# Optimization experiments

Hardware: AMD Instinct MI355X
Metric: run time of the kernel (lower is better)

Reference implementation:

```python
import jax, jax.numpy as jnp
import numpy as np
import math

B = 4096
D = 768
HID = 256
C_OLD = 100
C_NEW = 100
NUM_CLASSES = 200
EPSILON = 0.05
TAU = 0.1
EPS = 1e-8
NEG_INF = -1e9


def _l2_normalize(x):
    # matches F.normalize(p=2, dim=1, eps=1e-12)
    n = jnp.linalg.norm(x, axis=1, keepdims=True)
    return x / jnp.maximum(n, 1e-12)


def setup_inputs() -> dict:
    key = jax.random.key(0)
    k1, k2, k3, k4, k5, k6, k7 = jax.random.split(key, 7)
    z_u = jax.random.normal(k1, (B, D), dtype=jnp.float32)
    logits = jax.random.normal(k2, (B, NUM_CLASSES), dtype=jnp.float32)
    old_class_indices = jnp.arange(C_OLD, dtype=jnp.int64 if jax.config.jax_enable_x64 else jnp.int32)
    new_class_indices = jnp.arange(C_OLD, C_OLD + C_NEW, dtype=old_class_indices.dtype)
    base_features = jax.random.normal(k3, (B, D), dtype=jnp.float32)
    s = 1.0 / math.sqrt(D)
    f1_w = jax.random.uniform(k4, (HID, D), dtype=jnp.float32, minval=-s, maxval=s)
    f1_b = jax.random.uniform(k5, (HID,), dtype=jnp.float32, minval=-s, maxval=s)
    f2_w = jax.random.uniform(k6, (HID, D), dtype=jnp.float32, minval=-s, maxval=s)
    f2_b = jax.random.uniform(k7, (HID,), dtype=jnp.float32, minval=-s, maxval=s)
    return {"z_u": z_u, "logits": logits, "old_class_indices": old_class_indices,
            "new_class_indices": new_class_indices, "base_features": base_features,
            "f1_w": f1_w, "f1_b": f1_b, "f2_w": f2_w, "f2_b": f2_b}


def reference(z_u, logits, old_class_indices, new_class_indices, base_features,
              f1_w, f1_b, f2_w, f2_b):
    num_old = old_class_indices.shape[0]
    active = jnp.concatenate([old_class_indices, new_class_indices])

    # ---- soft entropy regularization ----
    probs = jax.nn.softmax(logits[:, active], axis=1)   # (B, C_old+C_new)
    mean_probs = probs.mean(axis=0)
    p_old = mean_probs[:num_old].sum()
    p_new = mean_probs[num_old:].sum()
    loss_inter = (p_old * jnp.log(p_old + EPS) + p_new * jnp.log(p_new + EPS)
                  + math.log(2.0))
    p_old_in = mean_probs[:num_old] / (p_old + EPS)
    loss_old_in = jnp.sum(p_old_in * jnp.log(p_old_in + EPS)) + math.log(num_old)
    p_new_in = mean_probs[num_old:] / (p_new + EPS)
    num_new = new_class_indices.shape[0]
    if num_new > 1:
        loss_new_in = jnp.sum(p_new_in * jnp.log(p_new_in + EPS)) + math.log(num_new)
    else:
        loss_new_in = jnp.float32(0.0)
    loss_entropy = loss_inter + loss_old_in + loss_new_in

    # ---- neighborhood mask from frozen base features ----
    base_norm = _l2_normalize(base_features)
    base_sim = base_norm @ base_norm.T                  # (B, B)
    eye = jnp.eye(base_sim.shape[0], dtype=bool)
    mask = (base_sim > EPSILON) & ~eye                  # (B, B) bool

    # ---- contrastive similarities ----
    z_norm = _l2_normalize(z_u)
    sim = z_norm @ z_norm.T                             # (B, B)

    f1_z = z_u @ f1_w.T + f1_b                          # (B, HID)
    f2_z = z_u @ f2_w.T + f2_b
    attn_logits = jnp.where(mask, f1_z @ f2_z.T, NEG_INF)
    w_ik = jax.nn.softmax(attn_logits, axis=1) * mask.astype(sim.dtype)

    exp_sim = jnp.where(eye, 0.0, jnp.exp(sim / TAU))
    denom = exp_sim.sum(axis=1, keepdims=True)
    log_prob = sim / TAU - jnp.log(denom + EPS)

    num_neighbors = mask.sum(axis=1).astype(sim.dtype)  # (B,)
    valid = num_neighbors > 0
    loss_i = -(w_ik * mask.astype(sim.dtype) * log_prob).sum(axis=1)
    per_sample = jnp.where(valid, loss_i / jnp.maximum(num_neighbors, 1.0), 0.0)
    n_valid = valid.sum().astype(sim.dtype)
    loss_contrastive = jnp.where(n_valid > 0,
                                 per_sample.sum() / jnp.maximum(n_valid, 1.0),
                                 0.0)

    total_loss = loss_entropy + loss_contrastive
    return total_loss
```

## Files before the change

### kernel.cpp

```cpp
#include <hip/hip_runtime.h>
#include <hip/hip_fp8.h>


#define B_N   4096
#define D_N   768
#define HID_N 256
#define NCLS  200

typedef __attribute__((ext_vector_type(8))) short v8s;
typedef __attribute__((ext_vector_type(4))) float v4f;

__device__ __forceinline__ unsigned short f2bf(float x) {
    unsigned int u = __float_as_uint(x);
    unsigned int r = (u + 0x7FFFu + ((u >> 16) & 1u)) >> 16;
    return (unsigned short)r;
}
__device__ __forceinline__ float bf2f(unsigned short h) {
    return __uint_as_float((unsigned int)h << 16);
}
__device__ __forceinline__ unsigned char f2fp8(float x) {
    __hip_fp8_e4m3 v(x);
    return (unsigned char)v.__x;
}

__device__ __forceinline__ void gld16c(const unsigned char* g, unsigned char* l) {
    __builtin_amdgcn_global_load_lds(
        (__attribute__((address_space(1))) void*)g,
        (__attribute__((address_space(3))) void*)l, 16, 0, 0);
}

#define ZERO_ACC(a) { _Pragma("unroll") for (int _i = 0; _i < 4; _i++) \
    _Pragma("unroll") for (int _j = 0; _j < 4; _j++) a[_i][_j] = (v4f){0.f,0.f,0.f,0.f}; }

__global__ __launch_bounds__(256) void pre_all(
    const float* __restrict__ z, const float* __restrict__ base,
    const float* __restrict__ w1, const float* __restrict__ w2,
    const float* __restrict__ b1, const float* __restrict__ b2,
    const float* __restrict__ logits, const int* __restrict__ oldi,
    const int* __restrict__ newi,
    unsigned char* __restrict__ zn8, unsigned char* __restrict__ bn8,
    unsigned char* __restrict__ f1z8, unsigned char* __restrict__ f2z8,
    float* __restrict__ mpart, float* __restrict__ accums)
{
    __shared__ __align__(16) unsigned char shmem[2 * 64 * 72 * 2];
    int tid = threadIdx.x;

    if (blockIdx.x < B_N) {
        float* ws1 = (float*)shmem;
        float* ws2 = ws1 + 4;
        int row = blockIdx.x;
        const float* zr = z    + (size_t)row * D_N;
        const float* br = base + (size_t)row * D_N;
        float z0 = zr[tid], z1 = zr[tid + 256], z2 = zr[tid + 512];
        float b0 = br[tid], b1v = br[tid + 256], b2v = br[tid + 512];
        float s1 = z0*z0 + z1*z1 + z2*z2;
        float s2 = b0*b0 + b1v*b1v + b2v*b2v;
        #pragma unroll
        for (int m = 32; m > 0; m >>= 1) { s1 += __shfl_xor(s1, m); s2 += __shfl_xor(s2, m); }
        if ((tid & 63) == 0) { ws1[tid >> 6] = s1; ws2[tid >> 6] = s2; }
        __syncthreads();
        float t1 = ws1[0] + ws1[1] + ws1[2] + ws1[3];
        float t2 = ws2[0] + ws2[1] + ws2[2] + ws2[3];
        float sc1 = 16.0f / fmaxf(sqrtf(t1), 1e-12f);
        float sc2 = 16.0f / fmaxf(sqrtf(t2), 1e-12f);
        size_t o = (size_t)row * D_N;
        int j0 = tid ^ (((row >> 3) & 1) << 3);
        zn8[o+j0] = f2fp8(z0*sc1);  zn8[o+j0+256] = f2fp8(z1*sc1);  zn8[o+j0+512] = f2fp8(z2*sc1);
        bn8[o+j0] = f2fp8(b0*sc2);  bn8[o+j0+256] = f2fp8(b1v*sc2); bn8[o+j0+512] = f2fp8(b2v*sc2);
        return;
    }
    if (blockIdx.x < B_N + 256) {
        int* act = (int*)shmem;
        float* accs = (float*)(shmem + 1024);
        int sb = blockIdx.x - B_N;
        int lane = tid & 63, wave = tid >> 6;
        if (sb == 0 && tid < 4) accums[tid] = 0.0f;
        if (tid < NCLS) act[tid] = (tid < 100) ? oldi[tid] : newi[tid - 100];
        accs[tid] = 0.f; accs[256 + tid] = 0.f; accs[512 + tid] = 0.f; accs[768 + tid] = 0.f;
        __syncthreads();
        int a0 = act[lane], a1 = act[lane + 64], a2 = act[lane + 128];
        int a3 = (lane < 8) ? act[lane + 192] : 0;
        int r0 = sb * 16 + wave * 4;
        float c0 = 0.f, c1 = 0.f, c2 = 0.f, c3 = 0.f;
        for (int i = 0; i < 4; i++) {
            const float* lr = logits + (size_t)(r0 + i) * NCLS;
            float x0 = lr[a0], x1 = lr[a1], x2 = lr[a2];
            float x3 = (lane < 8) ? lr[a3] : -3.0e38f;
            float m = fmaxf(fmaxf(x0, x1), fmaxf(x2, x3));
            #pragma unroll
            for (int s = 32; s > 0; s >>= 1) m = fmaxf(m, __shfl_xor(m, s));
            float e0 = __expf(x0 - m), e1 = __expf(x1 - m), e2 = __expf(x2 - m);
            float e3 = (lane < 8) ? __expf(x3 - m) : 0.f;
            float sm = e0 + e1 + e2 + e3;
            #pragma unroll
            for (int s = 32; s > 0; s >>= 1) sm += __shfl_xor(sm, s);
            float inv = 1.0f / sm;
            c0 += e0 * inv; c1 += e1 * inv; c2 += e2 * inv; c3 += e3 * inv;
        }
        accs[wave * 256 + lane] = c0; accs[wave * 256 + lane + 64] = c1;
        accs[wave * 256 + lane + 128] = c2;
        if (lane < 8) accs[wave * 256 + lane + 192] = c3;
        __syncthreads();
        mpart[(size_t)tid * 256 + sb] =
            accs[tid] + accs[256 + tid] + accs[512 + tid] + accs[768 + tid];
        return;
    }
    {
        unsigned short* Al = (unsigned short*)shmem;
        unsigned short* Bl = Al + 64 * 72;
        int f = blockIdx.x - (B_N + 256);
        int which = f >> 8;
        int t6 = f & 255;
        int mBase = (t6 >> 2) * 64;
        int nBase = (t6 & 3) * 64;
        const float* wsrc = which ? w2 : w1;
        const float* bias = which ? b2 : b1;
        unsigned char* outz = which ? f2z8 : f1z8;
        int lane = tid & 63, wave = tid >> 6, quad = lane >> 4, col = lane & 15;
        v4f acc[4];
        #pragma unroll
        for (int i = 0; i < 4; i++) acc[i] = (v4f){0.f, 0.f, 0.f, 0.f};
        for (int kc = 0; kc < D_N; kc += 64) {
            __syncthreads();
            #pragma unroll
            for (int s = 0; s < 4; s++) {
                int slot = s * 256 + tid;
                int row = slot >> 4, k4 = slot & 15;
                float4 va = *(const float4*)(z + (size_t)(mBase + row) * D_N + kc + k4 * 4);
                float4 vb = *(const float4*)(wsrc + (size_t)(nBase + row) * D_N + kc + k4 * 4);
                unsigned short* pa = Al + row * 72 + k4 * 4;
                unsigned short* pb = Bl + row * 72 + k4 * 4;
                pa[0] = f2bf(va.x); pa[1] = f2bf(va.y); pa[2] = f2bf(va.z); pa[3] = f2bf(va.w);
                pb[0] = f2bf(vb.x); pb[1] = f2bf(vb.y); pb[2] = f2bf(vb.z); pb[3] = f2bf(vb.w);
            }
            __syncthreads();
            #pragma unroll
            for (int kk = 0; kk < 2; kk++) {
                v8s af = *(const v8s*)(Al + (wave * 16 + col) * 72 + kk * 32 + quad * 8);
                #pragma unroll
                for (int tc = 0; tc < 4; tc++) {
                    v8s bf = *(const v8s*)(Bl + (tc * 16 + col) * 72 + kk * 32 + quad * 8);
                    acc[tc] = __builtin_amdgcn_mfma_f32_16x16x32_bf16(af, bf, acc[tc], 0, 0, 0);
                }
            }
        }
        #pragma unroll
        for (int tc = 0; tc < 4; tc++) {
            int gcol = nBase + tc * 16 + col;
            float bv = bias[gcol];
            #pragma unroll
            for (int reg = 0; reg < 4; reg++) {
                int grow = mBase + wave * 16 + quad * 4 + reg;
                int sw8 = ((grow >> 3) & 1) << 3;
                outz[(size_t)grow * HID_N + (gcol ^ sw8)] =
                    f2fp8(4.0f * (acc[tc][reg] + bv));
            }
        }
    }
}

__global__ __launch_bounds__(256, 2) void main_fused(
    const unsigned char* __restrict__ zn8, const unsigned char* __restrict__ bn8,
    const unsigned char* __restrict__ f1z8, const unsigned char* __restrict__ f2z8,
    float* __restrict__ partials)
{
    __shared__ __align__(16) unsigned char S[4 * 128 * 128];
    unsigned char* S0 = S;
    unsigned char* S1 = S + 1 * 128 * 128;
    unsigned char* S2 = S + 2 * 128 * 128;
    unsigned char* S3 = S + 3 * 128 * 128;
    int tid = threadIdx.x, lane = tid & 63, wave = tid >> 6, quad = lane >> 4, col = lane & 15;
    int wr = wave >> 1, wc = wave & 1;
    int ib = blockIdx.x, jc = blockIdx.y;
    int rBase = ib * 128 + wr * 64;
    int cBase = jc * 128 + wc * 64;
    const int r8 = lane >> 3;
    const int kbl8 = (lane & 7) ^ r8;
    const int sub8 = ((quad & 1) ^ (col >> 3)) << 3;

    v4f accB[4][4], accS[4][4];
    ZERO_ACC(accB); ZERO_ACC(accS);
    for (int kc = 0; kc < D_N; kc += 128) {
        __syncthreads();
        #pragma unroll
        for (int s = 0; s < 4; s++) {
            int rowbase = s * 32 + wave * 8;
            size_t rOff = (size_t)(ib * 128 + rowbase + r8) * D_N + kc + kbl8 * 16;
            size_t cOff = (size_t)(jc * 128 + rowbase + r8) * D_N + kc + kbl8 * 16;
            gld16c(bn8 + rOff, S0 + rowbase * 128);
            gld16c(bn8 + cOff, S1 + rowbase * 128);
            gld16c(zn8 + rOff, S2 + rowbase * 128);
            gld16c(zn8 + cOff, S3 + rowbase * 128);
        }
        __syncthreads();
        #pragma unroll
        for (int kk = 0; kk < 4; kk++) {
            int gbase = kk * 2 + (quad >> 1);
            int off = ((gbase ^ (col & 7)) << 4) + sub8;
            long a1[4], b1[4], a2[4], b2[4];
            #pragma unroll
            for (int t = 0; t < 4; t++) {
                int rA = (wr * 64 + t * 16 + col) * 128;
                int rB = (wc * 64 + t * 16 + col) * 128;
                a1[t] = *(const long*)(S0 + rA + off);
                b1[t] = *(const long*)(S1 + rB + off);
                a2[t] = *(const long*)(S2 + rA + off);
                b2[t] = *(const long*)(S3 + rB + off);
            }
            #pragma unroll
            for (int tr = 0; tr < 4; tr++)
                #pragma unroll
                for (int tc = 0; tc < 4; tc++) {
                    accB[tr][tc] = __builtin_amdgcn_mfma_f32_16x16x32_fp8_fp8(
                        a1[tr], b1[tc], accB[tr][tc], 0, 0, 0);
                    accS[tr][tc] = __builtin_amdgcn_mfma_f32_16x16x32_fp8_fp8(
                        a2[tr], b2[tc], accS[tr][tc], 0, 0, 0);
                }
        }
    }

    unsigned char* F1 = S0;
    unsigned char* F2 = S0 + 32768;
    __syncthreads();
    {
        int r4 = lane >> 4;
        #pragma unroll
        for (int s = 0; s < 8; s++) {
            int rowbase = s * 16 + wave * 4;
            int row = rowbase + r4;
            int kb = (lane & 15) ^ (row & 15);
            gld16c(f1z8 + (size_t)(ib * 128 + row) * HID_N + kb * 16, F1 + rowbase * 256);
            gld16c(f2z8 + (size_t)(jc * 128 + row) * HID_N + kb * 16, F2 + rowbase * 256);
        }
    }

    unsigned long long mb = 0ull;
    #pragma unroll
    for (int tr = 0; tr < 4; tr++)
        #pragma unroll
        for (int tc = 0; tc < 4; tc++)
            #pragma unroll
            for (int reg = 0; reg < 4; reg++) {
                int grow = rBase + tr * 16 + quad * 4 + reg;
                int gcol = cBase + tc * 16 + col;
                if (accB[tr][tc][reg] > 12.8f && grow != gcol)
                    mb |= 1ull << (tr * 16 + tc * 4 + reg);
            }

    float dsum[16];
    #pragma unroll
    for (int i = 0; i < 16; i++) dsum[i] = 0.f;
    unsigned int svp[4][4][2];
    #pragma unroll
    for (int tr = 0; tr < 4; tr++)
        #pragma unroll
        for (int tc = 0; tc < 4; tc++) {
            float s0 = accS[tr][tc][0] * 0.00390625f;
            float s1 = accS[tr][tc][1] * 0.00390625f;
            float s2 = accS[tr][tc][2] * 0.00390625f;
            float s3 = accS[tr][tc][3] * 0.00390625f;
            float svv[4] = {s0, s1, s2, s3};
            #pragma unroll
            for (int reg = 0; reg < 4; reg++) {
                int grow = rBase + tr * 16 + quad * 4 + reg;
                int gcol = cBase + tc * 16 + col;
                if (grow != gcol) dsum[tr * 4 + reg] += __expf(svv[reg] * 10.0f);
            }
            svp[tr][tc][0] = ((unsigned int)f2bf(s1) << 16) | f2bf(s0);
            svp[tr][tc][1] = ((unsigned int)f2bf(s3) << 16) | f2bf(s2);
        }

    v4f accA[4][4]; ZERO_ACC(accA);
    __syncthreads();
    #pragma unroll
    for (int kk = 0; kk < 8; kk++) {
        int gbase = kk * 2 + (quad >> 1);
        int off = ((gbase ^ col) << 4) + sub8;
        long af[4], bf[4];
        #pragma unroll
        for (int t = 0; t < 4; t++) {
            af[t] = *(const long*)(F1 + (wr * 64 + t * 16 + col) * 256 + off);
            bf[t] = *(const long*)(F2 + (wc * 64 + t * 16 + col) * 256 + off);
        }
        #pragma unroll
        for (int tr = 0; tr < 4; tr++)
            #pragma unroll
            for (int tc = 0; tc < 4; tc++)
                accA[tr][tc] = __builtin_amdgcn_mfma_f32_16x16x32_fp8_fp8(
                    af[tr], bf[tc], accA[tr][tc], 0, 0, 0);
    }

    float lsum[16], asum[16], nnf[16];
    #pragma unroll
    for (int i = 0; i < 16; i++) { lsum[i] = 0.f; asum[i] = 0.f; nnf[i] = 0.f; }
    #pragma unroll
    for (int tr = 0; tr < 4; tr++)
        #pragma unroll
        for (int tc = 0; tc < 4; tc++)
            #pragma unroll
            for (int reg = 0; reg < 4; reg++) {
                if ((mb >> (tr * 16 + tc * 4 + reg)) & 1ull) {
                    int slot = tr * 4 + reg;
                    float e = __expf(accA[tr][tc][reg] * 0.0625f);
                    unsigned int pk = svp[tr][tc][reg >> 1];
                    float sv = bf2f((unsigned short)((reg & 1) ? (pk >> 16) : (pk & 0xFFFF)));
                    lsum[slot] += e;
                    asum[slot] += e * sv;
                    nnf[slot] += 1.f;
                }
            }

    #pragma unroll
    for (int i = 0; i < 16; i++) {
        #pragma unroll
        for (int m = 1; m < 16; m <<= 1) {
            lsum[i] += __shfl_xor(lsum[i], m);
            asum[i] += __shfl_xor(asum[i], m);
            dsum[i] += __shfl_xor(dsum[i], m);
            nnf[i]  += __shfl_xor(nnf[i], m);
        }
        if (col == 0) {
            int row = rBase + (i >> 2) * 16 + quad * 4 + (i & 3);
            float4 v; v.x = lsum[i]; v.y = asum[i]; v.z = dsum[i]; v.w = nnf[i];
            *(float4*)(partials + ((size_t)row * 64 + jc * 2 + wc) * 4) = v;
        }
    }
}

__global__ __launch_bounds__(256) void row_reduce_fin(
    const float* __restrict__ partials, const float* __restrict__ mpart,
    float* __restrict__ acc, float* __restrict__ out)
{
    int tid = threadIdx.x;
    int row = blockIdx.x * 64 + (tid >> 2);
    int sub = tid & 3;
    const float4* p = (const float4*)partials + (size_t)row * 64 + sub * 16;
    float L = 0.f, A = 0.f, Dn = 0.f, NN = 0.f;
    #pragma unroll
    for (int c = 0; c < 16; c++) { float4 v = p[c]; L += v.x; A += v.y; Dn += v.z; NN += v.w; }
    #pragma unroll
    for (int m = 1; m < 4; m <<= 1) {
        L += __shfl_xor(L, m); A += __shfl_xor(A, m);
        Dn += __shfl_xor(Dn, m); NN += __shfl_xor(NN, m);
    }
    float per = 0.f, val = 0.f;
    if (sub == 0 && NN > 0.5f) {
        per = (logf(Dn + 1e-8f) - 10.0f * (A / L)) / NN;
        val = 1.0f;
    }
    __shared__ float red[256];
    __shared__ float r2s[256];
    __shared__ int amLast;
    red[tid] = per; r2s[tid] = val; __syncthreads();
    for (int s = 128; s > 0; s >>= 1) {
        if (tid < s) { red[tid] += red[tid + s]; r2s[tid] += r2s[tid + s]; }
        __syncthreads();
    }
    if (tid == 0) {
        atomicAdd(&acc[0], red[0]);
        atomicAdd(&acc[1], r2s[0]);
        __threadfence();
        int old = atomicAdd((int*)&acc[2], 1);
        amLast = (old == (int)gridDim.x - 1);
    }
    __syncthreads();
    if (!amLast) return;

    __shared__ float bcast[2];
    float pcl = 0.0f;
    if (tid < NCLS) {
        const float4* mp = (const float4*)(mpart + (size_t)tid * 256);
        float s = 0.f;
        #pragma unroll
        for (int c = 0; c < 64; c++) { float4 v = mp[c]; s += v.x + v.y + v.z + v.w; }
        pcl = s * (1.0f / 4096.0f);
    }
    red[tid] = (tid < 100) ? pcl : 0.0f; __syncthreads();
    for (int s = 128; s > 0; s >>= 1) { if (tid < s) red[tid] += red[tid + s]; __syncthreads(); }
    if (tid == 0) bcast[0] = red[0];
    __syncthreads();
    red[tid] = (tid >= 100 && tid < NCLS) ? pcl : 0.0f; __syncthreads();
    for (int s = 128; s > 0; s >>= 1) { if (tid < s) red[tid] += red[tid + s]; __syncthreads(); }
    if (tid == 0) bcast[1] = red[0];
    __syncthreads();
    float p_old = bcast[0], p_new = bcast[1];

    float t = 0.0f;
    if (tid < 100)       { float q = pcl / (p_old + 1e-8f); t = q * logf(q + 1e-8f); }
    else if (tid < NCLS) { float q = pcl / (p_new + 1e-8f); t = q * logf(q + 1e-8f); }
    red[tid] = t; __syncthreads();
    for (int s = 128; s > 0; s >>= 1) { if (tid < s) red[tid] += red[tid + s]; __syncthreads(); }

    if (tid == 0) {
        float s0 = __hip_atomic_load(&acc[0], __ATOMIC_RELAXED, __HIP_MEMORY_SCOPE_AGENT);
        float s1 = __hip_atomic_load(&acc[1], __ATOMIC_RELAXED, __HIP_MEMORY_SCOPE_AGENT);
        float loss_inter = p_old * logf(p_old + 1e-8f) + p_new * logf(p_new + 1e-8f)
                           + 0.69314718056f;
        float loss_entropy = loss_inter + red[0] + 2.0f * 4.60517018599f;
        float lc = (s1 > 0.5f) ? s0 / s1 : 0.0f;
        out[0] = loss_entropy + lc;
    }
}

extern "C" void kernel_launch(void* const* d_in, const int* in_sizes, int n_in,
                              void* d_out, int out_size, void* d_ws, size_t ws_size,
                              hipStream_t stream)
{
    const float* z_u    = (const float*)d_in[0];
    const float* logits = (const float*)d_in[1];
    const int*   oldi   = (const int*)d_in[2];
    const int*   newi   = (const int*)d_in[3];
    const float* basef  = (const float*)d_in[4];
    const float* f1w    = (const float*)d_in[5];
    const float* f1b    = (const float*)d_in[6];
    const float* f2w    = (const float*)d_in[7];
    const float* f2b    = (const float*)d_in[8];
    float* out = (float*)d_out;

    unsigned char* zn8   = (unsigned char*)d_ws;
    unsigned char* bn8   = zn8 + (size_t)B_N * D_N;
    unsigned char* f1z8  = bn8 + (size_t)B_N * D_N;
    unsigned char* f2z8  = f1z8 + (size_t)B_N * HID_N;
    float* partials = (float*)(f2z8 + (size_t)B_N * HID_N);
    float* mpart    = partials + (size_t)B_N * 64 * 4;
    float* accums   = mpart + 256 * 256;

    pre_all<<<B_N + 256 + 512, 256, 0, stream>>>(
        z_u, basef, f1w, f2w, f1b, f2b, logits, oldi, newi,
        zn8, bn8, f1z8, f2z8, mpart, accums);
    main_fused<<<dim3(32, 32), 256, 0, stream>>>(zn8, bn8, f1z8, f2z8, partials);
    row_reduce_fin<<<64, 256, 0, stream>>>(partials, mpart, accums, out);
}
```

Before: 177.4 us.

## Fuse row reduction and finalization into main kernel via atomics and last-block

Removes the separate row_reduce_fin kernel. main_fused now accumulates per-row statistics directly with global atomicAdd into a zeroed rowacc buffer, which pre_all clears. The last block to finish, found with an atomic counter, then computes the contrastive and entropy terms. This saves a kernel launch and the partials round-trip through memory, but adds many contended atomics (64 per row) and a serial final reduction over 4096 rows inside a single block.

Result: slower. 277.9 us (+56.7%).

```diff
diff --git a/kernel.cpp b/kernel.cpp
--- a/kernel.cpp
+++ b/kernel.cpp
@@ -40,7 +40,8 @@
     const int* __restrict__ newi,
     unsigned char* __restrict__ zn8, unsigned char* __restrict__ bn8,
     unsigned char* __restrict__ f1z8, unsigned char* __restrict__ f2z8,
-    float* __restrict__ mpart, float* __restrict__ accums)
+    float* __restrict__ mpart, float* __restrict__ rowacc,
+    float* __restrict__ accums)
 {
     __shared__ __align__(16) unsigned char shmem[2 * 64 * 72 * 2];
     int tid = threadIdx.x;
@@ -49,6 +50,7 @@
         float* ws1 = (float*)shmem;
         float* ws2 = ws1 + 4;
         int row = blockIdx.x;
+        if (tid == 0) *(float4*)(rowacc + (size_t)row * 4) = make_float4(0.f, 0.f, 0.f, 0.f);
         const float* zr = z    + (size_t)row * D_N;
         const float* br = base + (size_t)row * D_N;
         float z0 = zr[tid], z1 = zr[tid + 256], z2 = zr[tid + 512];
@@ -162,7 +164,8 @@
 __global__ __launch_bounds__(256, 2) void main_fused(
     const unsigned char* __restrict__ zn8, const unsigned char* __restrict__ bn8,
     const unsigned char* __restrict__ f1z8, const unsigned char* __restrict__ f2z8,
-    float* __restrict__ partials)
+    float* __restrict__ rowacc, const float* __restrict__ mpart,
+    float* __restrict__ accums, float* __restrict__ out)
 {
     __shared__ __align__(16) unsigned char S[4 * 128 * 128];
     unsigned char* S0 = S;
@@ -321,52 +324,47 @@
         }
         if (col == 0) {
             int row = rBase + (i >> 2) * 16 + quad * 4 + (i & 3);
-            float4 v; v.x = lsum[i]; v.y = asum[i]; v.z = dsum[i]; v.w = nnf[i];
-            *(float4*)(partials + ((size_t)row * 64 + jc * 2 + wc) * 4) = v;
-        }
-    }
-}
-
-__global__ __launch_bounds__(256) void row_reduce_fin(
-    const float* __restrict__ partials, const float* __restrict__ mpart,
-    float* __restrict__ acc, float* __restrict__ out)
-{
-    int tid = threadIdx.x;
-    int row = blockIdx.x * 64 + (tid >> 2);
-    int sub = tid & 3;
-    const float4* p = (const float4*)partials + (size_t)row * 64 + sub * 16;
-    float L = 0.f, A = 0.f, Dn = 0.f, NN = 0.f;
-    #pragma unroll
-    for (int c = 0; c < 16; c++) { float4 v = p[c]; L += v.x; A += v.y; Dn += v.z; NN += v.w; }
-    #pragma unroll
-    for (int m = 1; m < 4; m <<= 1) {
-        L += __shfl_xor(L, m); A += __shfl_xor(A, m);
-        Dn += __shfl_xor(Dn, m); NN += __shfl_xor(NN, m);
-    }
-    float per = 0.f, val = 0.f;
-    if (sub == 0 && NN > 0.5f) {
-        per = (logf(Dn + 1e-8f) - 10.0f * (A / L)) / NN;
-        val = 1.0f;
-    }
-    __shared__ float red[256];
-    __shared__ float r2s[256];
+            float* rp = rowacc + (size_t)row * 4;
+            atomicAdd(rp + 0, lsum[i]);
+            atomicAdd(rp + 1, asum[i]);
+            atomicAdd(rp + 2, dsum[i]);
+            atomicAdd(rp + 3, nnf[i]);
+        }
+    }
+
+    __threadfence();
     __shared__ int amLast;
-    red[tid] = per; r2s[tid] = val; __syncthreads();
+    if (tid == 0) {
+        int old = atomicAdd((int*)&accums[2], 1);
+        amLast = (old == (int)(gridDim.x * gridDim.y) - 1);
+    }
+    __syncthreads();
+    if (!amLast) return;
+
+    float* red = (float*)S;
+    float* r2s = red + 256;
+
+    float lsumT = 0.f, cntT = 0.f;
+    for (int k = 0; k < 16; k++) {
+        int row = tid + k * 256;
+        float* rp = rowacc + (size_t)row * 4;
+        float L  = __hip_atomic_load(rp + 0, __ATOMIC_RELAXED, __HIP_MEMORY_SCOPE_AGENT);
+        float A  = __hip_atomic_load(rp + 1, __ATOMIC_RELAXED, __HIP_MEMORY_SCOPE_AGENT);
+        float Dn = __hip_atomic_load(rp + 2, __ATOMIC_RELAXED, __HIP_MEMORY_SCOPE_AGENT);
+        float NN = __hip_atomic_load(rp + 3, __ATOMIC_RELAXED, __HIP_MEMORY_SCOPE_AGENT);
+        if (NN > 0.5f) {
+            lsumT += (logf(Dn + 1e-8f) - 10.0f * (A / L)) / NN;
+            cntT += 1.f;
+        }
+    }
+    red[tid] = lsumT; r2s[tid] = cntT; __syncthreads();
     for (int s = 128; s > 0; s >>= 1) {
         if (tid < s) { red[tid] += red[tid + s]; r2s[tid] += r2s[tid + s]; }
         __syncthreads();
     }
-    if (tid == 0) {
-        atomicAdd(&acc[0], red[0]);
-        atomicAdd(&acc[1], r2s[0]);
-        __threadfence();
-        int old = atomicAdd((int*)&acc[2], 1);
-        amLast = (old == (int)gridDim.x - 1);
-    }
+    float lcn = red[0], lcd = r2s[0];
     __syncthreads();
-    if (!amLast) return;
-
-    __shared__ float bcast[2];
+
     float pcl = 0.0f;
     if (tid < NCLS) {
         const float4* mp = (const float4*)(mpart + (size_t)tid * 256);
@@ -377,13 +375,10 @@
     }
     red[tid] = (tid < 100) ? pcl : 0.0f; __syncthreads();
     for (int s = 128; s > 0; s >>= 1) { if (tid < s) red[tid] += red[tid + s]; __syncthreads(); }
-    if (tid == 0) bcast[0] = red[0];
-    __syncthreads();
+    float p_old = red[0]; __syncthreads();
     red[tid] = (tid >= 100 && tid < NCLS) ? pcl : 0.0f; __syncthreads();
     for (int s = 128; s > 0; s >>= 1) { if (tid < s) red[tid] += red[tid + s]; __syncthreads(); }
-    if (tid == 0) bcast[1] = red[0];
-    __syncthreads();
-    float p_old = bcast[0], p_new = bcast[1];
+    float p_new = red[0]; __syncthreads();
 
     float t = 0.0f;
     if (tid < 100)       { float q = pcl / (p_old + 1e-8f); t = q * logf(q + 1e-8f); }
@@ -392,12 +387,10 @@
     for (int s = 128; s > 0; s >>= 1) { if (tid < s) red[tid] += red[tid + s]; __syncthreads(); }
 
     if (tid == 0) {
-        float s0 = __hip_atomic_load(&acc[0], __ATOMIC_RELAXED, __HIP_MEMORY_SCOPE_AGENT);
-        float s1 = __hip_atomic_load(&acc[1], __ATOMIC_RELAXED, __HIP_MEMORY_SCOPE_AGENT);
         float loss_inter = p_old * logf(p_old + 1e-8f) + p_new * logf(p_new + 1e-8f)
                            + 0.69314718056f;
         float loss_entropy = loss_inter + red[0] + 2.0f * 4.60517018599f;
-        float lc = (s1 > 0.5f) ? s0 / s1 : 0.0f;
+        float lc = (lcd > 0.5f) ? lcn / lcd : 0.0f;
         out[0] = loss_entropy + lc;
     }
 }
@@ -421,13 +414,13 @@
     unsigned char* bn8   = zn8 + (size_t)B_N * D_N;
     unsigned char* f1z8  = bn8 + (size_t)B_N * D_N;
     unsigned char* f2z8  = f1z8 + (size_t)B_N * HID_N;
-    float* partials = (float*)(f2z8 + (size_t)B_N * HID_N);
-    float* mpart    = partials + (size_t)B_N * 64 * 4;
-    float* accums   = mpart + 256 * 256;
+    float* rowacc = (float*)(f2z8 + (size_t)B_N * HID_N);
+    float* mpart  = rowacc + (size_t)B_N * 4;
+    float* accums = mpart + 256 * 256;
 
     pre_all<<<B_N + 256 + 512, 256, 0, stream>>>(
         z_u, basef, f1w, f2w, f1b, f2b, logits, oldi, newi,
-        zn8, bn8, f1z8, f2z8, mpart, accums);
-    main_fused<<<dim3(32, 32), 256, 0, stream>>>(zn8, bn8, f1z8, f2z8, partials);
-    row_reduce_fin<<<64, 256, 0, stream>>>(partials, mpart, accums, out);
-}
+        zn8, bn8, f1z8, f2z8, mpart, rowacc, accums);
+    main_fused<<<dim3(32, 32), 256, 0, stream>>>(zn8, bn8, f1z8, f2z8,
+                                                 rowacc, mpart, accums, out);
+}
```
